# Kernel tuning notes

Hardware: AMD Instinct MI355X
Metric: run time of the kernel (lower is better)

## Reference

```python
import jax, jax.numpy as jnp
import numpy as np

N_NODES = 50000
N_EDGES = 800000
IN_DIM = 256
HID_DIM = 256
OUT_DIM = 2


def setup_inputs() -> dict:
    key = jax.random.key(0)
    ks = jax.random.split(key, 8)
    x = jax.random.normal(ks[0], (N_NODES, IN_DIM), dtype=jnp.float32)
    edge_index = jax.random.randint(ks[1], (2, N_EDGES), 0, N_NODES, dtype=jnp.int64)
    # GCNConv weights (PyG: out = norm_agg(x @ W) + b), Glorot-ish scale
    W1 = jax.random.normal(ks[2], (IN_DIM, HID_DIM), dtype=jnp.float32) / np.sqrt(IN_DIM)
    b1 = jnp.zeros((HID_DIM,), dtype=jnp.float32)
    W2 = jax.random.normal(ks[3], (HID_DIM, HID_DIM), dtype=jnp.float32) / np.sqrt(HID_DIM)
    b2 = jnp.zeros((HID_DIM,), dtype=jnp.float32)
    Wfc = jax.random.normal(ks[4], (HID_DIM, OUT_DIM), dtype=jnp.float32) / np.sqrt(HID_DIM)
    bfc = jnp.zeros((OUT_DIM,), dtype=jnp.float32)
    return {"x": x, "edge_index": edge_index, "W1": W1, "b1": b1,
            "W2": W2, "b2": b2, "Wfc": Wfc, "bfc": bfc}


def _edge_norm(edge_index, n_nodes):
    # GCNConv: add self-loops, symmetric normalization D^-1/2 A_hat D^-1/2
    loop = jnp.arange(n_nodes, dtype=edge_index.dtype)
    src = jnp.concatenate([edge_index[0], loop])  # [E+N]
    dst = jnp.concatenate([edge_index[1], loop])  # [E+N]
    deg = jax.ops.segment_sum(jnp.ones_like(dst, dtype=jnp.float32), dst,
                              num_segments=n_nodes)
    dis = jnp.where(deg > 0, jax.lax.rsqrt(deg), 0.0)  # deg_inv_sqrt [N]
    norm = dis[src] * dis[dst]  # [E+N]
    return src, dst, norm


def _gcn_layer(x, W, b, src, dst, norm, n_nodes):
    h = x @ W  # [N, F_out]
    msg = h[src] * norm[:, None]  # gather + scale, [E+N, F_out]
    return jax.ops.segment_sum(msg, dst, num_segments=n_nodes) + b


def reference(x, edge_index, W1, b1, W2, b2, Wfc, bfc):
    n = x.shape[0]
    src, dst, norm = _edge_norm(edge_index, n)
    h = jax.nn.relu(_gcn_layer(x, W1, b1, src, dst, norm, n))
    # dropout is identity in eval mode
    h = jax.nn.relu(_gcn_layer(h, W2, b2, src, dst, norm, n))
    logits = h @ Wfc + bfc
    return jax.nn.log_softmax(logits, axis=1)
```

## Files before the change

### kernel.cpp

```cpp
#include <hip/hip_runtime.h>
#include <math.h>

#define N_NODES 50000
#define N_EDGES 800000
#define DIM 256
#define SCAN_BLOCKS ((N_NODES + 255) / 256)
#define NXBLK 12500
#define NDEGBLK ((N_EDGES + 255) / 256)

typedef short bf16x8 __attribute__((ext_vector_type(8)));
typedef float f32x4 __attribute__((ext_vector_type(4)));

__device__ __forceinline__ float bf2f(unsigned short u) {
    return __uint_as_float(((unsigned)u) << 16);
}
__device__ __forceinline__ unsigned short f2bf(float f) {
    unsigned u = __float_as_uint(f);
    return (unsigned short)((u + 0x7fffu + ((u >> 16) & 1u)) >> 16);
}

__global__ __launch_bounds__(256) void k_prep(const float* __restrict__ x,
                                              unsigned short* __restrict__ xb,
                                              const float* __restrict__ W1,
                                              unsigned short* __restrict__ W1t,
                                              const float* __restrict__ W2,
                                              unsigned short* __restrict__ W2t,
                                              const int* __restrict__ dst,
                                              int* __restrict__ ideg,
                                              int* __restrict__ erank) {
    int bid = blockIdx.x;
    int tid = threadIdx.x;
    if (bid < NXBLK) {
        int i = bid * 256 + tid;
        float4 v = ((const float4*)x)[i];
        ((ushort4*)xb)[i] = make_ushort4(f2bf(v.x), f2bf(v.y), f2bf(v.z), f2bf(v.w));
    } else if (bid < NXBLK + 256) {
        int n = bid - NXBLK;
        W1t[n * 256 + tid] = f2bf(W1[tid * 256 + n]);
    } else if (bid < NXBLK + 512) {
        int n = bid - NXBLK - 256;
        W2t[n * 256 + tid] = f2bf(W2[tid * 256 + n]);
    } else {
        int e = (bid - NXBLK - 512) * 256 + tid;
        if (e < N_EDGES) erank[e] = atomicAdd(&ideg[dst[e]], 1);
    }
}


__global__ __launch_bounds__(256) void k_scan_block(const int* __restrict__ ideg,
                                                    int* __restrict__ rowptr,
                                                    int* __restrict__ blocksum) {
    __shared__ int s[256];
    int t = threadIdx.x;
    int i = blockIdx.x * 256 + t;
    int v = (i < N_NODES) ? ideg[i] : 0;
    s[t] = v;
    for (int off = 1; off < 256; off <<= 1) {
        __syncthreads();
        int add = (t >= off) ? s[t - off] : 0;
        __syncthreads();
        s[t] += add;
    }
    __syncthreads();
    if (i < N_NODES) rowptr[i] = s[t] - v;
    if (t == 255) blocksum[blockIdx.x] = s[255];
}

__global__ __launch_bounds__(256) void k_scan_add(int* __restrict__ rowptr,
                                                  const int* __restrict__ blocksum,
                                                  const int* __restrict__ ideg,
                                                  float* __restrict__ dis) {
    __shared__ int s[256];
    int t = threadIdx.x;
    int v = (t < SCAN_BLOCKS) ? blocksum[t] : 0;
    s[t] = v;
    for (int off = 1; off < 256; off <<= 1) {
        __syncthreads();
        int add = (t >= off) ? s[t - off] : 0;
        __syncthreads();
        s[t] += add;
    }
    __syncthreads();
    int excl = s[t] - v;
    __syncthreads();
    s[t] = excl;
    __syncthreads();
    int off = s[blockIdx.x];

    int i = blockIdx.x * 256 + t;
    if (i < N_NODES) {
        rowptr[i] += off;
        dis[i] = rsqrtf((float)(ideg[i] + 1));
    }
    if (i == 0) rowptr[N_NODES] = N_EDGES;
}

__global__ void k_csr_fill(const int* __restrict__ src, const int* __restrict__ dst,
                           const int* __restrict__ erank,
                           const int* __restrict__ rowptr,
                           unsigned long long* __restrict__ csr_pk,
                           const float* __restrict__ dis) {
    int e = blockIdx.x * blockDim.x + threadIdx.x;
    if (e < N_EDGES) {
        int s = src[e];
        int pos = rowptr[dst[e]] + erank[e];
        csr_pk[pos] = (unsigned)s |
            ((unsigned long long)__float_as_uint(dis[s]) << 32);
    }
}

__global__ __launch_bounds__(256) void k_agg_bf16(const unsigned short* __restrict__ in,
                                                  const float* __restrict__ dis,
                                                  const int* __restrict__ rowptr,
                                                  const unsigned long long* __restrict__ csr_pk,
                                                  unsigned short* __restrict__ out) {
    int node = blockIdx.x * 4 + (threadIdx.x >> 6);
    if (node >= N_NODES) return;
    int lane = threadIdx.x & 63;
    int f = lane * 4;

    float dn = dis[node];
    ushort4 sv = *(const ushort4*)(in + (size_t)node * DIM + f);
    float a0 = dn * bf2f(sv.x);
    float a1 = dn * bf2f(sv.y);
    float a2 = dn * bf2f(sv.z);
    float a3 = dn * bf2f(sv.w);

    int e = rowptr[node];
    int eEnd = rowptr[node + 1];
    for (; e + 3 < eEnd; e += 4) {
        unsigned long long p0 = csr_pk[e],     p1 = csr_pk[e + 1];
        unsigned long long p2 = csr_pk[e + 2], p3 = csr_pk[e + 3];
        int s0 = (int)(unsigned)p0, s1 = (int)(unsigned)p1;
        int s2 = (int)(unsigned)p2, s3 = (int)(unsigned)p3;
        float w0 = __uint_as_float((unsigned)(p0 >> 32));
        float w1 = __uint_as_float((unsigned)(p1 >> 32));
        float w2 = __uint_as_float((unsigned)(p2 >> 32));
        float w3 = __uint_as_float((unsigned)(p3 >> 32));
        ushort4 v0 = *(const ushort4*)(in + (size_t)s0 * DIM + f);
        ushort4 v1 = *(const ushort4*)(in + (size_t)s1 * DIM + f);
        ushort4 v2 = *(const ushort4*)(in + (size_t)s2 * DIM + f);
        ushort4 v3 = *(const ushort4*)(in + (size_t)s3 * DIM + f);
        a0 += w0 * bf2f(v0.x) + w1 * bf2f(v1.x) + w2 * bf2f(v2.x) + w3 * bf2f(v3.x);
        a1 += w0 * bf2f(v0.y) + w1 * bf2f(v1.y) + w2 * bf2f(v2.y) + w3 * bf2f(v3.y);
        a2 += w0 * bf2f(v0.z) + w1 * bf2f(v1.z) + w2 * bf2f(v2.z) + w3 * bf2f(v3.z);
        a3 += w0 * bf2f(v0.w) + w1 * bf2f(v1.w) + w2 * bf2f(v2.w) + w3 * bf2f(v3.w);
    }
    for (; e < eEnd; ++e) {
        unsigned long long p0 = csr_pk[e];
        int s0 = (int)(unsigned)p0;
        float w0 = __uint_as_float((unsigned)(p0 >> 32));
        ushort4 v0 = *(const ushort4*)(in + (size_t)s0 * DIM + f);
        a0 += w0 * bf2f(v0.x);
        a1 += w0 * bf2f(v0.y);
        a2 += w0 * bf2f(v0.z);
        a3 += w0 * bf2f(v0.w);
    }
    a0 *= dn; a1 *= dn; a2 *= dn; a3 *= dn;
    *(ushort4*)(out + (size_t)node * DIM + f) =
        make_ushort4(f2bf(a0), f2bf(a1), f2bf(a2), f2bf(a3));
}

__global__ __launch_bounds__(256) void k_gemm_wide(const unsigned short* __restrict__ A,
                                                   const unsigned short* __restrict__ Wt,
                                                   const float* __restrict__ bias,
                                                   unsigned short* __restrict__ C, int M) {
    __shared__ unsigned short As[4][64][8];
    __shared__ unsigned short Bs[4][256][8];

    int tid = threadIdx.x;
    int lane = tid & 63;
    int wave = tid >> 6;
    int lr = lane & 15;
    int lc = lane >> 4;

    int rowBase = blockIdx.x * 64;

    f32x4 acc[16] = {};

    int r = tid >> 2;
    int c = tid & 3;

    for (int k0 = 0; k0 < DIM; k0 += 32) {
        float4 z = make_float4(0.f, 0.f, 0.f, 0.f);
        int gr0 = rowBase + r;
        float4 va0 = (gr0 < M) ? *(const float4*)(A + (size_t)gr0 * DIM + k0 + c * 8) : z;
        *(float4*)&As[c][r][0] = va0;
#pragma unroll
        for (int jj = 0; jj < 4; ++jj) {
            int brow = r + 64 * jj;
            *(float4*)&Bs[c][brow][0] = *(const float4*)(Wt + (size_t)brow * DIM + k0 + c * 8);
        }
        __syncthreads();

        bf16x8 af = *(const bf16x8*)&As[lc][wave * 16 + lr][0];
#pragma unroll
        for (int n = 0; n < 16; ++n) {
            bf16x8 bfr = *(const bf16x8*)&Bs[lc][n * 16 + lr][0];
            acc[n] = __builtin_amdgcn_mfma_f32_16x16x32_bf16(af, bfr, acc[n], 0, 0, 0);
        }
        __syncthreads();
    }

    float bv[16];
#pragma unroll
    for (int n = 0; n < 16; ++n) bv[n] = bias[n * 16 + lr];

#pragma unroll
    for (int reg = 0; reg < 4; ++reg) {
        int row = rowBase + wave * 16 + lc * 4 + reg;
        if (row < M) {
#pragma unroll
            for (int n = 0; n < 16; ++n) {
                float v = fmaxf(acc[n][reg] + bv[n], 0.f);
                C[(size_t)row * DIM + n * 16 + lr] = f2bf(v);
            }
        }
    }
}

__global__ __launch_bounds__(256) void k_gemm_fc(const unsigned short* __restrict__ A,
                                                 const unsigned short* __restrict__ Wt,
                                                 const float* __restrict__ bias,
                                                 const float* __restrict__ Wfc,
                                                 const float* __restrict__ bfc,
                                                 float* __restrict__ out, int M) {
    __shared__ unsigned short As[4][64][8];
    __shared__ unsigned short Bs[4][256][8];

    int tid = threadIdx.x;
    int lane = tid & 63;
    int wave = tid >> 6;
    int lr = lane & 15;
    int lc = lane >> 4;

    int rowBase = blockIdx.x * 64;

    f32x4 acc[16] = {};

    int r = tid >> 2;
    int c = tid & 3;

    for (int k0 = 0; k0 < DIM; k0 += 32) {
        float4 z = make_float4(0.f, 0.f, 0.f, 0.f);
        int gr0 = rowBase + r;
        float4 va0 = (gr0 < M) ? *(const float4*)(A + (size_t)gr0 * DIM + k0 + c * 8) : z;
        *(float4*)&As[c][r][0] = va0;
#pragma unroll
        for (int jj = 0; jj < 4; ++jj) {
            int brow = r + 64 * jj;
            *(float4*)&Bs[c][brow][0] = *(const float4*)(Wt + (size_t)brow * DIM + k0 + c * 8);
        }
        __syncthreads();

        bf16x8 af = *(const bf16x8*)&As[lc][wave * 16 + lr][0];
#pragma unroll
        for (int n = 0; n < 16; ++n) {
            bf16x8 bfr = *(const bf16x8*)&Bs[lc][n * 16 + lr][0];
            acc[n] = __builtin_amdgcn_mfma_f32_16x16x32_bf16(af, bfr, acc[n], 0, 0, 0);
        }
        __syncthreads();
    }

    float bv[16], wf0[16], wf1[16];
#pragma unroll
    for (int n = 0; n < 16; ++n) {
        int col = n * 16 + lr;
        bv[n]  = bias[col];
        wf0[n] = Wfc[col * 2 + 0];
        wf1[n] = Wfc[col * 2 + 1];
    }
    float bb0 = bfc[0], bb1 = bfc[1];

#pragma unroll
    for (int reg = 0; reg < 4; ++reg) {
        int row = rowBase + wave * 16 + lc * 4 + reg;
        float s0 = 0.f, s1 = 0.f;
#pragma unroll
        for (int n = 0; n < 16; ++n) {
            float v = fmaxf(acc[n][reg] + bv[n], 0.f);
            s0 += v * wf0[n];
            s1 += v * wf1[n];
        }
#pragma unroll
        for (int o = 1; o < 16; o <<= 1) {
            s0 += __shfl_xor(s0, o);
            s1 += __shfl_xor(s1, o);
        }
        if (lr == 0 && row < M) {
            float l0 = s0 + bb0;
            float l1 = s1 + bb1;
            float mx = fmaxf(l0, l1);
            float lse = mx + logf(expf(l0 - mx) + expf(l1 - mx));
            out[(size_t)row * 2 + 0] = l0 - lse;
            out[(size_t)row * 2 + 1] = l1 - lse;
        }
    }
}

extern "C" void kernel_launch(void* const* d_in, const int* in_sizes, int n_in,
                              void* d_out, int out_size, void* d_ws, size_t ws_size,
                              hipStream_t stream) {
    const float* x      = (const float*)d_in[0];
    const int* ei       = (const int*)d_in[1];
    const int* esrc     = ei;
    const int* edst     = ei + N_EDGES;
    const float* W1  = (const float*)d_in[2];
    const float* b1  = (const float*)d_in[3];
    const float* W2  = (const float*)d_in[4];
    const float* b2  = (const float*)d_in[5];
    const float* Wfc = (const float*)d_in[6];
    const float* bfc = (const float*)d_in[7];
    float* out = (float*)d_out;

    const size_t NF = (size_t)N_NODES * DIM;
    unsigned short* P0 = (unsigned short*)d_ws;
    unsigned short* P1 = P0 + NF;
    unsigned short* P2 = P1 + NF;
    unsigned short* W1t = P2 + NF;
    unsigned short* W2t = W1t + 256 * 256;
    unsigned long long* csr_pk = (unsigned long long*)(W2t + 256 * 256);
    float* dis    = (float*)(csr_pk + N_EDGES);
    int* ideg     = (int*)(dis + N_NODES);
    int* rowptr   = ideg + N_NODES;
    int* erank    = rowptr + N_NODES + 1;
    int* blocksum = erank + N_EDGES;

    (void)hipMemsetAsync(ideg, 0, N_NODES * sizeof(int), stream);
    k_prep<<<NXBLK + 512 + NDEGBLK, 256, 0, stream>>>(x, P0, W1, W1t, W2, W2t, edst, ideg, erank);
    k_scan_block<<<SCAN_BLOCKS, 256, 0, stream>>>(ideg, rowptr, blocksum);
    k_scan_add<<<SCAN_BLOCKS, 256, 0, stream>>>(rowptr, blocksum, ideg, dis);
    k_csr_fill<<<(N_EDGES + 255) / 256, 256, 0, stream>>>(esrc, edst, erank, rowptr, csr_pk, dis);

    int aggBlocks = (N_NODES + 3) / 4;
    int gemmBlocks = (N_NODES + 63) / 64;

    k_agg_bf16<<<aggBlocks, 256, 0, stream>>>(P0, dis, rowptr, csr_pk, P1);
    k_gemm_wide<<<gemmBlocks, 256, 0, stream>>>(P1, W1t, b1, P2, N_NODES);

    k_agg_bf16<<<aggBlocks, 256, 0, stream>>>(P2, dis, rowptr, csr_pk, P0);
    k_gemm_fc<<<gemmBlocks, 256, 0, stream>>>(P0, W2t, b2, Wfc, bfc, out, N_NODES);
}
```

Measured before the change: 250.5 us.

## Reorder GCN to transform-then-aggregate and fuse CSR fill, bias, and FC head

Each GCN layer now runs the GEMM before aggregation, matching the reference order. This lets bias and ReLU move into the aggregation epilogue, and the second aggregation folds in the final FC plus log-softmax with a wave reduction. The CSR fill is merged into the first GEMM launch as extra blocks, so the edge scatter and dense matmul run in one grid, and one launch is dropped. In exchange, the fused head reduces across 64 lanes for every node, and bf16 rounding now happens at different points.

```diff
diff --git a/kernel.cpp b/kernel.cpp
--- a/kernel.cpp
+++ b/kernel.cpp
@@ -7,6 +7,7 @@
 #define SCAN_BLOCKS ((N_NODES + 255) / 256)
 #define NXBLK 12500
 #define NDEGBLK ((N_EDGES + 255) / 256)
+#define GEMM_BLK ((N_NODES + 63) / 64)
 
 typedef short bf16x8 __attribute__((ext_vector_type(8)));
 typedef float f32x4 __attribute__((ext_vector_type(4)));
@@ -95,29 +96,134 @@
     if (i == 0) rowptr[N_NODES] = N_EDGES;
 }
 
-__global__ void k_csr_fill(const int* __restrict__ src, const int* __restrict__ dst,
-                           const int* __restrict__ erank,
-                           const int* __restrict__ rowptr,
-                           unsigned long long* __restrict__ csr_pk,
-                           const float* __restrict__ dis) {
-    int e = blockIdx.x * blockDim.x + threadIdx.x;
-    if (e < N_EDGES) {
-        int s = src[e];
-        int pos = rowptr[dst[e]] + erank[e];
-        csr_pk[pos] = (unsigned)s |
-            ((unsigned long long)__float_as_uint(dis[s]) << 32);
-    }
-}
-
-__global__ __launch_bounds__(256) void k_agg_bf16(const unsigned short* __restrict__ in,
-                                                  const float* __restrict__ dis,
-                                                  const int* __restrict__ rowptr,
-                                                  const unsigned long long* __restrict__ csr_pk,
-                                                  unsigned short* __restrict__ out) {
+__global__ __launch_bounds__(256) void k_mega(const unsigned short* __restrict__ A,
+                                              const unsigned short* __restrict__ Wt,
+                                              unsigned short* __restrict__ Y,
+                                              const int* __restrict__ src,
+                                              const int* __restrict__ dst,
+                                              const int* __restrict__ erank,
+                                              const int* __restrict__ rowptr,
+                                              unsigned long long* __restrict__ csr_pk,
+                                              const float* __restrict__ dis) {
+    __shared__ unsigned short As[4][64][8];
+    __shared__ unsigned short Bs[4][256][8];
+
+    int bid = blockIdx.x;
+    int tid = threadIdx.x;
+
+    if (bid >= GEMM_BLK) {
+        int e = (bid - GEMM_BLK) * 256 + tid;
+        if (e < N_EDGES) {
+            int s = src[e];
+            int pos = rowptr[dst[e]] + erank[e];
+            csr_pk[pos] = (unsigned)s |
+                ((unsigned long long)__float_as_uint(dis[s]) << 32);
+        }
+        return;
+    }
+
+    int lane = tid & 63;
+    int wave = tid >> 6;
+    int lr = lane & 15;
+    int lc = lane >> 4;
+    int rowBase = bid * 64;
+
+    f32x4 acc[16] = {};
+    int r = tid >> 2;
+    int c = tid & 3;
+
+    for (int k0 = 0; k0 < DIM; k0 += 32) {
+        float4 z = make_float4(0.f, 0.f, 0.f, 0.f);
+        int gr0 = rowBase + r;
+        float4 va0 = (gr0 < N_NODES) ? *(const float4*)(A + (size_t)gr0 * DIM + k0 + c * 8) : z;
+        *(float4*)&As[c][r][0] = va0;
+#pragma unroll
+        for (int jj = 0; jj < 4; ++jj) {
+            int brow = r + 64 * jj;
+            *(float4*)&Bs[c][brow][0] = *(const float4*)(Wt + (size_t)brow * DIM + k0 + c * 8);
+        }
+        __syncthreads();
+
+        bf16x8 af = *(const bf16x8*)&As[lc][wave * 16 + lr][0];
+#pragma unroll
+        for (int n = 0; n < 16; ++n) {
+            bf16x8 bfr = *(const bf16x8*)&Bs[lc][n * 16 + lr][0];
+            acc[n] = __builtin_amdgcn_mfma_f32_16x16x32_bf16(af, bfr, acc[n], 0, 0, 0);
+        }
+        __syncthreads();
+    }
+
+#pragma unroll
+    for (int reg = 0; reg < 4; ++reg) {
+        int row = rowBase + wave * 16 + lc * 4 + reg;
+        if (row < N_NODES) {
+#pragma unroll
+            for (int n = 0; n < 16; ++n)
+                Y[(size_t)row * DIM + n * 16 + lr] = f2bf(acc[n][reg]);
+        }
+    }
+}
+
+__global__ __launch_bounds__(256) void k_gemm_plain(const unsigned short* __restrict__ A,
+                                                    const unsigned short* __restrict__ Wt,
+                                                    unsigned short* __restrict__ Y, int M) {
+    __shared__ unsigned short As[4][64][8];
+    __shared__ unsigned short Bs[4][256][8];
+
+    int tid = threadIdx.x;
+    int lane = tid & 63;
+    int wave = tid >> 6;
+    int lr = lane & 15;
+    int lc = lane >> 4;
+    int rowBase = blockIdx.x * 64;
+
+    f32x4 acc[16] = {};
+    int r = tid >> 2;
+    int c = tid & 3;
+
+    for (int k0 = 0; k0 < DIM; k0 += 32) {
+        float4 z = make_float4(0.f, 0.f, 0.f, 0.f);
+        int gr0 = rowBase + r;
+        float4 va0 = (gr0 < M) ? *(const float4*)(A + (size_t)gr0 * DIM + k0 + c * 8) : z;
+        *(float4*)&As[c][r][0] = va0;
+#pragma unroll
+        for (int jj = 0; jj < 4; ++jj) {
+            int brow = r + 64 * jj;
+            *(float4*)&Bs[c][brow][0] = *(const float4*)(Wt + (size_t)brow * DIM + k0 + c * 8);
+        }
+        __syncthreads();
+
+        bf16x8 af = *(const bf16x8*)&As[lc][wave * 16 + lr][0];
+#pragma unroll
+        for (int n = 0; n < 16; ++n) {
+            bf16x8 bfr = *(const bf16x8*)&Bs[lc][n * 16 + lr][0];
+            acc[n] = __builtin_amdgcn_mfma_f32_16x16x32_bf16(af, bfr, acc[n], 0, 0, 0);
+        }
+        __syncthreads();
+    }
+
+#pragma unroll
+    for (int reg = 0; reg < 4; ++reg) {
+        int row = rowBase + wave * 16 + lc * 4 + reg;
+        if (row < M) {
+#pragma unroll
+            for (int n = 0; n < 16; ++n)
+                Y[(size_t)row * DIM + n * 16 + lr] = f2bf(acc[n][reg]);
+        }
+    }
+}
+
+__global__ __launch_bounds__(256) void k_agg_l1(const unsigned short* __restrict__ in,
+                                                const float* __restrict__ dis,
+                                                const int* __restrict__ rowptr,
+                                                const unsigned long long* __restrict__ csr_pk,
+                                                const float* __restrict__ bias,
+                                                unsigned short* __restrict__ out) {
     int node = blockIdx.x * 4 + (threadIdx.x >> 6);
     if (node >= N_NODES) return;
     int lane = threadIdx.x & 63;
     int f = lane * 4;
+    float4 bv = *(const float4*)(bias + f);
 
     float dn = dis[node];
     ushort4 sv = *(const ushort4*)(in + (size_t)node * DIM + f);
@@ -156,145 +262,86 @@
         a2 += w0 * bf2f(v0.z);
         a3 += w0 * bf2f(v0.w);
     }
-    a0 *= dn; a1 *= dn; a2 *= dn; a3 *= dn;
+    a0 = fmaxf(a0 * dn + bv.x, 0.f);
+    a1 = fmaxf(a1 * dn + bv.y, 0.f);
+    a2 = fmaxf(a2 * dn + bv.z, 0.f);
+    a3 = fmaxf(a3 * dn + bv.w, 0.f);
     *(ushort4*)(out + (size_t)node * DIM + f) =
         make_ushort4(f2bf(a0), f2bf(a1), f2bf(a2), f2bf(a3));
 }
 
-__global__ __launch_bounds__(256) void k_gemm_wide(const unsigned short* __restrict__ A,
-                                                   const unsigned short* __restrict__ Wt,
-                                                   const float* __restrict__ bias,
-                                                   unsigned short* __restrict__ C, int M) {
-    __shared__ unsigned short As[4][64][8];
-    __shared__ unsigned short Bs[4][256][8];
-
-    int tid = threadIdx.x;
-    int lane = tid & 63;
-    int wave = tid >> 6;
-    int lr = lane & 15;
-    int lc = lane >> 4;
-
-    int rowBase = blockIdx.x * 64;
-
-    f32x4 acc[16] = {};
-
-    int r = tid >> 2;
-    int c = tid & 3;
-
-    for (int k0 = 0; k0 < DIM; k0 += 32) {
-        float4 z = make_float4(0.f, 0.f, 0.f, 0.f);
-        int gr0 = rowBase + r;
-        float4 va0 = (gr0 < M) ? *(const float4*)(A + (size_t)gr0 * DIM + k0 + c * 8) : z;
-        *(float4*)&As[c][r][0] = va0;
-#pragma unroll
-        for (int jj = 0; jj < 4; ++jj) {
-            int brow = r + 64 * jj;
-            *(float4*)&Bs[c][brow][0] = *(const float4*)(Wt + (size_t)brow * DIM + k0 + c * 8);
-        }
-        __syncthreads();
-
-        bf16x8 af = *(const bf16x8*)&As[lc][wave * 16 + lr][0];
-#pragma unroll
-        for (int n = 0; n < 16; ++n) {
-            bf16x8 bfr = *(const bf16x8*)&Bs[lc][n * 16 + lr][0];
-            acc[n] = __builtin_amdgcn_mfma_f32_16x16x32_bf16(af, bfr, acc[n], 0, 0, 0);
-        }
-        __syncthreads();
-    }
-
-    float bv[16];
-#pragma unroll
-    for (int n = 0; n < 16; ++n) bv[n] = bias[n * 16 + lr];
-
-#pragma unroll
-    for (int reg = 0; reg < 4; ++reg) {
-        int row = rowBase + wave * 16 + lc * 4 + reg;
-        if (row < M) {
-#pragma unroll
-            for (int n = 0; n < 16; ++n) {
-                float v = fmaxf(acc[n][reg] + bv[n], 0.f);
-                C[(size_t)row * DIM + n * 16 + lr] = f2bf(v);
-            }
-        }
-    }
-}
-
-__global__ __launch_bounds__(256) void k_gemm_fc(const unsigned short* __restrict__ A,
-                                                 const unsigned short* __restrict__ Wt,
-                                                 const float* __restrict__ bias,
-                                                 const float* __restrict__ Wfc,
-                                                 const float* __restrict__ bfc,
-                                                 float* __restrict__ out, int M) {
-    __shared__ unsigned short As[4][64][8];
-    __shared__ unsigned short Bs[4][256][8];
-
-    int tid = threadIdx.x;
-    int lane = tid & 63;
-    int wave = tid >> 6;
-    int lr = lane & 15;
-    int lc = lane >> 4;
-
-    int rowBase = blockIdx.x * 64;
-
-    f32x4 acc[16] = {};
-
-    int r = tid >> 2;
-    int c = tid & 3;
-
-    for (int k0 = 0; k0 < DIM; k0 += 32) {
-        float4 z = make_float4(0.f, 0.f, 0.f, 0.f);
-        int gr0 = rowBase + r;
-        float4 va0 = (gr0 < M) ? *(const float4*)(A + (size_t)gr0 * DIM + k0 + c * 8) : z;
-        *(float4*)&As[c][r][0] = va0;
-#pragma unroll
-        for (int jj = 0; jj < 4; ++jj) {
-            int brow = r + 64 * jj;
-            *(float4*)&Bs[c][brow][0] = *(const float4*)(Wt + (size_t)brow * DIM + k0 + c * 8);
-        }
-        __syncthreads();
-
-        bf16x8 af = *(const bf16x8*)&As[lc][wave * 16 + lr][0];
-#pragma unroll
-        for (int n = 0; n < 16; ++n) {
-            bf16x8 bfr = *(const bf16x8*)&Bs[lc][n * 16 + lr][0];
-            acc[n] = __builtin_amdgcn_mfma_f32_16x16x32_bf16(af, bfr, acc[n], 0, 0, 0);
-        }
-        __syncthreads();
-    }
-
-    float bv[16], wf0[16], wf1[16];
-#pragma unroll
-    for (int n = 0; n < 16; ++n) {
-        int col = n * 16 + lr;
-        bv[n]  = bias[col];
-        wf0[n] = Wfc[col * 2 + 0];
-        wf1[n] = Wfc[col * 2 + 1];
-    }
+__global__ __launch_bounds__(256) void k_agg_l2fc(const unsigned short* __restrict__ in,
+                                                  const float* __restrict__ dis,
+                                                  const int* __restrict__ rowptr,
+                                                  const unsigned long long* __restrict__ csr_pk,
+                                                  const float* __restrict__ bias,
+                                                  const float* __restrict__ Wfc,
+                                                  const float* __restrict__ bfc,
+                                                  float* __restrict__ out) {
+    int node = blockIdx.x * 4 + (threadIdx.x >> 6);
+    if (node >= N_NODES) return;
+    int lane = threadIdx.x & 63;
+    int f = lane * 4;
+    float4 bv = *(const float4*)(bias + f);
+    float4 wfa = *(const float4*)(Wfc + f * 2);
+    float4 wfb = *(const float4*)(Wfc + f * 2 + 4);
     float bb0 = bfc[0], bb1 = bfc[1];
 
-#pragma unroll
-    for (int reg = 0; reg < 4; ++reg) {
-        int row = rowBase + wave * 16 + lc * 4 + reg;
-        float s0 = 0.f, s1 = 0.f;
-#pragma unroll
-        for (int n = 0; n < 16; ++n) {
-            float v = fmaxf(acc[n][reg] + bv[n], 0.f);
-            s0 += v * wf0[n];
-            s1 += v * wf1[n];
-        }
-#pragma unroll
-        for (int o = 1; o < 16; o <<= 1) {
-            s0 += __shfl_xor(s0, o);
-            s1 += __shfl_xor(s1, o);
-        }
-        if (lr == 0 && row < M) {
-            float l0 = s0 + bb0;
-            float l1 = s1 + bb1;
-            float mx = fmaxf(l0, l1);
-            float lse = mx + logf(expf(l0 - mx) + expf(l1 - mx));
-            out[(size_t)row * 2 + 0] = l0 - lse;
-            out[(size_t)row * 2 + 1] = l1 - lse;
-        }
+    float dn = dis[node];
+    ushort4 sv = *(const ushort4*)(in + (size_t)node * DIM + f);
+    float a0 = dn * bf2f(sv.x);
+    float a1 = dn * bf2f(sv.y);
+    float a2 = dn * bf2f(sv.z);
+    float a3 = dn * bf2f(sv.w);
+
+    int e = rowptr[node];
+    int eEnd = rowptr[node + 1];
+    for (; e + 3 < eEnd; e += 4) {
+        unsigned long long p0 = csr_pk[e],     p1 = csr_pk[e + 1];
+        unsigned long long p2 = csr_pk[e + 2], p3 = csr_pk[e + 3];
+        int s0 = (int)(unsigned)p0, s1 = (int)(unsigned)p1;
+        int s2 = (int)(unsigned)p2, s3 = (int)(unsigned)p3;
+        float w0 = __uint_as_float((unsigned)(p0 >> 32));
+        float w1 = __uint_as_float((unsigned)(p1 >> 32));
+        float w2 = __uint_as_float((unsigned)(p2 >> 32));
+        float w3 = __uint_as_float((unsigned)(p3 >> 32));
+        ushort4 v0 = *(const ushort4*)(in + (size_t)s0 * DIM + f);
+        ushort4 v1 = *(const ushort4*)(in + (size_t)s1 * DIM + f);
+        ushort4 v2 = *(const ushort4*)(in + (size_t)s2 * DIM + f);
+        ushort4 v3 = *(const ushort4*)(in + (size_t)s3 * DIM + f);
+        a0 += w0 * bf2f(v0.x) + w1 * bf2f(v1.x) + w2 * bf2f(v2.x) + w3 * bf2f(v3.x);
+        a1 += w0 * bf2f(v0.y) + w1 * bf2f(v1.y) + w2 * bf2f(v2.y) + w3 * bf2f(v3.y);
+        a2 += w0 * bf2f(v0.z) + w1 * bf2f(v1.z) + w2 * bf2f(v2.z) + w3 * bf2f(v3.z);
+        a3 += w0 * bf2f(v0.w) + w1 * bf2f(v1.w) + w2 * bf2f(v2.w) + w3 * bf2f(v3.w);
+    }
+    for (; e < eEnd; ++e) {
+        unsigned long long p0 = csr_pk[e];
+        int s0 = (int)(unsigned)p0;
+        float w0 = __uint_as_float((unsigned)(p0 >> 32));
+        ushort4 v0 = *(const ushort4*)(in + (size_t)s0 * DIM + f);
+        a0 += w0 * bf2f(v0.x);
+        a1 += w0 * bf2f(v0.y);
+        a2 += w0 * bf2f(v0.z);
+        a3 += w0 * bf2f(v0.w);
+    }
+    float h0 = fmaxf(a0 * dn + bv.x, 0.f);
+    float h1 = fmaxf(a1 * dn + bv.y, 0.f);
+    float h2 = fmaxf(a2 * dn + bv.z, 0.f);
+    float h3 = fmaxf(a3 * dn + bv.w, 0.f);
+    float s0 = h0 * wfa.x + h1 * wfa.z + h2 * wfb.x + h3 * wfb.z;
+    float s1 = h0 * wfa.y + h1 * wfa.w + h2 * wfb.y + h3 * wfb.w;
+#pragma unroll
+    for (int o = 1; o < 64; o <<= 1) {
+        s0 += __shfl_xor(s0, o);
+        s1 += __shfl_xor(s1, o);
+    }
+    if (lane == 0) {
+        float l0 = s0 + bb0;
+        float l1 = s1 + bb1;
+        float mx = fmaxf(l0, l1);
+        float lse = mx + logf(expf(l0 - mx) + expf(l1 - mx));
+        out[(size_t)node * 2 + 0] = l0 - lse;
+        out[(size_t)node * 2 + 1] = l1 - lse;
     }
 }
 
@@ -330,14 +377,14 @@
     k_prep<<<NXBLK + 512 + NDEGBLK, 256, 0, stream>>>(x, P0, W1, W1t, W2, W2t, edst, ideg, erank);
     k_scan_block<<<SCAN_BLOCKS, 256, 0, stream>>>(ideg, rowptr, blocksum);
     k_scan_add<<<SCAN_BLOCKS, 256, 0, stream>>>(rowptr, blocksum, ideg, dis);
-    k_csr_fill<<<(N_EDGES + 255) / 256, 256, 0, stream>>>(esrc, edst, erank, rowptr, csr_pk, dis);
+
+    k_mega<<<GEMM_BLK + NDEGBLK, 256, 0, stream>>>(P0, W1t, P1,
+                                                   esrc, edst, erank, rowptr, csr_pk, dis);
 
     int aggBlocks = (N_NODES + 3) / 4;
-    int gemmBlocks = (N_NODES + 63) / 64;
-
-    k_agg_bf16<<<aggBlocks, 256, 0, stream>>>(P0, dis, rowptr, csr_pk, P1);
-    k_gemm_wide<<<gemmBlocks, 256, 0, stream>>>(P1, W1t, b1, P2, N_NODES);
-
-    k_agg_bf16<<<aggBlocks, 256, 0, stream>>>(P2, dis, rowptr, csr_pk, P0);
-    k_gemm_fc<<<gemmBlocks, 256, 0, stream>>>(P0, W2t, b2, Wfc, bfc, out, N_NODES);
-}
+
+    k_agg_l1<<<aggBlocks, 256, 0, stream>>>(P1, dis, rowptr, csr_pk, b1, P2);
+
+    k_gemm_plain<<<GEMM_BLK, 256, 0, stream>>>(P2, W2t, P0, N_NODES);
+    k_agg_l2fc<<<aggBlocks, 256, 0, stream>>>(P0, dis, rowptr, csr_pk, b2, Wfc, bfc, out);
+}
```

Measured after the change: 236.0 us. 5.8% less time.
